# Optimization experiments

Hardware: AMD Instinct MI355X
Metric: run time of the kernel (lower is better)

Reference implementation:

```python
import jax, jax.numpy as jnp
import numpy as np


def setup_inputs() -> dict:
    key = jax.random.key(0)
    k1, k2, k3 = jax.random.split(key, 3)
    B, V, J = 32, 100000, 52
    vertices = jax.random.normal(k1, (1, V, 3), dtype=jnp.float32)
    lbs_weights = jax.random.uniform(k2, (1, V, J), dtype=jnp.float32)
    skinning_transforms = jax.random.normal(k3, (B, J, 4, 4), dtype=jnp.float32)
    return {
        "vertices": vertices,
        "lbs_weights": lbs_weights,
        "skinning_transforms": skinning_transforms,
    }


def reference(vertices, lbs_weights, skinning_transforms):
    # 3D-vertices branch of Skinning.forward
    B = skinning_transforms.shape[0]
    J = skinning_transforms.shape[1]
    V = vertices.shape[1]
    # W: [B,V,J] (broadcast of [1,V,J]); T_flat: [B,V,16] -> T: [B,V,4,4]
    T = jnp.einsum(
        "bvj,bjx->bvx",
        jnp.broadcast_to(lbs_weights, (B, V, J)),
        skinning_transforms.reshape(B, J, 16),
    ).reshape(B, V, 4, 4)
    # homogeneous vertex coords [B,V,4]
    v_posed_homo = jnp.concatenate(
        [
            jnp.broadcast_to(vertices, (B, V, 3)),
            jnp.ones((B, V, 1), dtype=vertices.dtype),
        ],
        axis=2,
    )
    # per-vertex 4x4 @ 4 transform, keep xyz
    v_homo = jnp.einsum("bvij,bvj->bvi", T, v_posed_homo)
    return v_homo[:, :, :3]
```

## Files before the change

### kernel.cpp

```cpp
#include <hip/hip_runtime.h>
#include <hip/hip_bf16.h>


typedef __attribute__((ext_vector_type(8))) short bf16x8;
typedef __attribute__((ext_vector_type(4))) float f32x4;

constexpr int J      = 52;
constexpr int KSTEPS = 7;
constexpr int NT     = 6;
constexpr int WAVES  = 4;
constexpr int MT     = 2;
constexpr int VPW    = MT * 16;
constexpr int VPB    = WAVES * VPW;

constexpr int SLOTS_FULL = 6 * NT * 64;
constexpr int SLOTS_S6   = NT * 32;
constexpr int ZSLOT      = SLOTS_FULL + SLOTS_S6;
constexpr int NSLOT      = ZSLOT + 1;
constexpr int S6_BASE_B  = SLOTS_FULL * 16;
constexpr int Z_B        = ZSLOT * 16;
constexpr int LDS_B      = 40960;

typedef const __attribute__((address_space(1))) char* gas1_t;
typedef __attribute__((address_space(3))) char* las3_t;

__device__ __forceinline__ unsigned pk2(float a, float b) {
    __hip_bfloat162 h = __float22bfloat162_rn(make_float2(a, b));
    return *reinterpret_cast<unsigned*>(&h);
}

__global__ __launch_bounds__(256) void pack_A(
    const float* __restrict__ xf,
    bf16x8* __restrict__ Bp)
{
    const int slot = blockIdx.x * 256 + threadIdx.x;
    if (slot >= NSLOT) return;

    if (slot == ZSLOT) {
        union { bf16x8 v; unsigned w[4]; } z;
        z.w[0] = z.w[1] = z.w[2] = z.w[3] = 0u;
        Bp[slot] = z.v;
        return;
    }

    int s, t, l;
    if (slot < SLOTS_FULL) {
        s = slot / (NT * 64);
        const int rem = slot - s * (NT * 64);
        t = rem >> 6;
        l = rem & 63;
    } else {
        s = 6;
        const int rem = slot - SLOTS_FULL;
        t = rem >> 5;
        l = rem & 31;
    }
    const int lgrp = l >> 4;
    const int lrow = l & 15;
    const int n = t * 16 + lrow;
    const int b = n / 3;
    const int i = n - 3 * b;
    const int j0 = s * 8 + lgrp * 2;

    const float4* __restrict__ xf4 = reinterpret_cast<const float4*>(xf);
    const float4 m0 = xf4[(b * J + j0) * 4 + i];
    const float4 m1 = xf4[(b * J + j0 + 1) * 4 + i];
    union { bf16x8 v; unsigned w[4]; } r;
    r.w[0] = pk2(m0.x, m0.y); r.w[1] = pk2(m0.z, m0.w);
    r.w[2] = pk2(m1.x, m1.y); r.w[3] = pk2(m1.z, m1.w);
    Bp[slot] = r.v;
}

__global__ __launch_bounds__(256, 4) void skin_mfma(
    const float* __restrict__ verts,
    const float* __restrict__ weights,
    const bf16x8* __restrict__ Bp,
    float* __restrict__ out,
    int V)
{
    __shared__ __align__(16) char sBp[LDS_B];

    const int tid  = threadIdx.x;
    const int lane = tid & 63;
    const int wid  = tid >> 6;
    const int lgrp = lane >> 4;
    const int lrow = lane & 15;
    const int v0   = blockIdx.x * VPB;

    {
        const char* g = (const char*)Bp;
        for (int p = wid; p < LDS_B / 1024; p += WAVES) {
            __builtin_amdgcn_global_load_lds(
                (gas1_t)(g + p * 1024 + lane * 16),
                (las3_t)(sBp + p * 1024), 16, 0, 0);
        }
    }

    int   vv[MT];
    bool  vok[MT];
    float hx[MT], hy[MT], hz[MT];
    float2 wv[MT][KSTEPS];
#pragma unroll
    for (int mt = 0; mt < MT; ++mt) {
        const int v = v0 + wid * VPW + mt * 16 + lrow;
        vv[mt]  = v;
        vok[mt] = (v < V);
        const int vcl = vok[mt] ? v : (V - 1);
        hx[mt] = verts[3 * (size_t)vcl + 0];
        hy[mt] = verts[3 * (size_t)vcl + 1];
        hz[mt] = verts[3 * (size_t)vcl + 2];
        const float* wr = weights + (size_t)vcl * J;
#pragma unroll
        for (int s = 0; s < KSTEPS; ++s) {
            const int j0 = s * 8 + lgrp * 2;
            wv[mt][s] = (j0 < J) ? *(const float2*)(wr + j0) : float2{0.f, 0.f};
        }
    }

    __syncthreads();

    f32x4 acc[MT][NT];
#pragma unroll
    for (int mt = 0; mt < MT; ++mt)
#pragma unroll
        for (int t = 0; t < NT; ++t)
            acc[mt][t] = f32x4{0.f, 0.f, 0.f, 0.f};

#pragma unroll
    for (int s = 0; s < KSTEPS; ++s) {
        bf16x8 frag[NT];
#pragma unroll
        for (int t = 0; t < NT; ++t) {
            if (s < 6) {
                frag[t] = *(const bf16x8*)(sBp + ((s * NT + t) * 64 + lane) * 16);
            } else {
                const char* p = (lane < 32)
                    ? (sBp + S6_BASE_B + (t * 32 + lane) * 16)
                    : (sBp + Z_B);
                frag[t] = *(const bf16x8*)p;
            }
        }
#pragma unroll
        for (int mt = 0; mt < MT; ++mt) {
            const float w0 = wv[mt][s].x, w1 = wv[mt][s].y;
            union { bf16x8 v; unsigned w[4]; } xf8;
            xf8.w[0] = pk2(w0 * hx[mt], w0 * hy[mt]);
            xf8.w[1] = pk2(w0 * hz[mt], w0);
            xf8.w[2] = pk2(w1 * hx[mt], w1 * hy[mt]);
            xf8.w[3] = pk2(w1 * hz[mt], w1);
#pragma unroll
            for (int t = 0; t < NT; ++t) {
                acc[mt][t] = __builtin_amdgcn_mfma_f32_16x16x32_bf16(
                    frag[t], xf8.v, acc[mt][t], 0, 0, 0);
            }
        }
    }

#pragma unroll
    for (int mt = 0; mt < MT; ++mt) {
        if (!vok[mt]) continue;
        const size_t v3 = (size_t)vv[mt] * 3;
#pragma unroll
        for (int t = 0; t < NT; ++t) {
#pragma unroll
            for (int r = 0; r < 4; ++r) {
                const int n = 16 * t + lgrp * 4 + r;
                const int b = n / 3;
                const int i = n - 3 * b;
                out[(size_t)b * (size_t)V * 3 + v3 + i] = acc[mt][t][r];
            }
        }
    }
}

extern "C" void kernel_launch(void* const* d_in, const int* in_sizes, int n_in,
                              void* d_out, int out_size, void* d_ws, size_t ws_size,
                              hipStream_t stream)
{
    const float* verts   = (const float*)d_in[0];
    const float* weights = (const float*)d_in[1];
    const float* xf      = (const float*)d_in[2];
    float* out = (float*)d_out;

    const int V = in_sizes[0] / 3;
    bf16x8* Bp = (bf16x8*)d_ws;

    pack_A<<<(NSLOT + 255) / 256, 256, 0, stream>>>(xf, Bp);
    const int nblocks = (V + VPB - 1) / VPB;
    skin_mfma<<<nblocks, 256, 0, stream>>>(verts, weights, Bp, out, V);
}
```

Measured before the change: 28.70 us.

## Stage MFMA outputs through LDS for coalesced float4 global stores

The epilogue used to write each accumulator element as a scattered scalar store. It now writes each wave's results into a per-wave LDS slice, transposed so that the 32 vertices × 3 coords for each batch form a contiguous run. It then reads them back as float4 and issues coalesced 16-byte global stores, in two halves of 16 batches each. This targets output write efficiency, which dominates a memory-bound kernel, at the cost of an extra block barrier, LDS round trips and manual waitcnt/sched barriers.

```diff
diff --git a/kernel.cpp b/kernel.cpp
--- a/kernel.cpp
+++ b/kernel.cpp
@@ -20,6 +20,7 @@
 constexpr int S6_BASE_B  = SLOTS_FULL * 16;
 constexpr int Z_B        = ZSLOT * 16;
 constexpr int LDS_B      = 40960;
+constexpr int SL_B       = 16 * VPW * 3 * 4;
 
 typedef const __attribute__((address_space(1))) char* gas1_t;
 typedef __attribute__((address_space(3))) char* las3_t;
@@ -86,6 +87,7 @@
     const int lgrp = lane >> 4;
     const int lrow = lane & 15;
     const int v0   = blockIdx.x * VPB;
+    const int v0w  = v0 + wid * VPW;
 
     {
         const char* g = (const char*)Bp;
@@ -96,16 +98,12 @@
         }
     }
 
-    int   vv[MT];
-    bool  vok[MT];
     float hx[MT], hy[MT], hz[MT];
     float2 wv[MT][KSTEPS];
 #pragma unroll
     for (int mt = 0; mt < MT; ++mt) {
-        const int v = v0 + wid * VPW + mt * 16 + lrow;
-        vv[mt]  = v;
-        vok[mt] = (v < V);
-        const int vcl = vok[mt] ? v : (V - 1);
+        const int v   = v0w + mt * 16 + lrow;
+        const int vcl = (v < V) ? v : (V - 1);
         hx[mt] = verts[3 * (size_t)vcl + 0];
         hy[mt] = verts[3 * (size_t)vcl + 1];
         hz[mt] = verts[3 * (size_t)vcl + 2];
@@ -156,18 +154,53 @@
         }
     }
 
-#pragma unroll
-    for (int mt = 0; mt < MT; ++mt) {
-        if (!vok[mt]) continue;
-        const size_t v3 = (size_t)vv[mt] * 3;
-#pragma unroll
-        for (int t = 0; t < NT; ++t) {
-#pragma unroll
-            for (int r = 0; r < 4; ++r) {
-                const int n = 16 * t + lgrp * 4 + r;
-                const int b = n / 3;
-                const int i = n - 3 * b;
-                out[(size_t)b * (size_t)V * 3 + v3 + i] = acc[mt][t][r];
+    __syncthreads();
+
+    char* const sl = sBp + wid * SL_B;
+    const long long validf = ((long long)V - v0w) * 3;
+#pragma unroll
+    for (int h = 0; h < 2; ++h) {
+#pragma unroll
+        for (int mt = 0; mt < MT; ++mt) {
+            const int vloc = mt * 16 + lrow;
+#pragma unroll
+            for (int tt = 0; tt < 3; ++tt) {
+                const int t = 3 * h + tt;
+#pragma unroll
+                for (int r = 0; r < 4; ++r) {
+                    const int n  = 16 * t + lgrp * 4 + r;
+                    const int b  = n / 3;
+                    const int i  = n - 3 * b;
+                    const int fl = ((b - 16 * h) * VPW + vloc) * 3 + i;
+                    *(float*)(sl + fl * 4) = acc[mt][t][r];
+                }
+            }
+        }
+        asm volatile("s_waitcnt lgkmcnt(0)" ::: "memory");
+        __builtin_amdgcn_sched_barrier(0);
+
+        f32x4 vals[6];
+#pragma unroll
+        for (int q = 0; q < 6; ++q) {
+            const int f = q * 64 + lane;
+            vals[q] = *(const f32x4*)(sl + f * 16);
+        }
+        asm volatile("s_waitcnt lgkmcnt(0)" ::: "memory");
+        __builtin_amdgcn_sched_barrier(0);
+
+#pragma unroll
+        for (int q = 0; q < 6; ++q) {
+            const int f  = q * 64 + lane;
+            const int bl = f / 24;
+            const int rr = f - bl * 24;
+            float* dst = out + (size_t)(16 * h + bl) * (size_t)V * 3
+                             + (size_t)v0w * 3 + rr * 4;
+            if ((long long)(rr + 1) * 4 <= validf) {
+                *(float4*)dst = *(const float4*)&vals[q];
+            } else if ((long long)rr * 4 < validf) {
+#pragma unroll
+                for (int e = 0; e < 4; ++e)
+                    if ((long long)(rr * 4 + e) < validf) dst[e] = vals[q][e];
             }
         }
     }
```

New measurement: 23.84 us, median of 3. -16.9%, faster.
